# Performance work log

Measured on AMD Instinct MI355X. Metric: run time of the kernel, lower is better.

## Reference

```python
import jax, jax.numpy as jnp
import numpy as np

B, N, BS, H, DH, L, FF, V, R = 1, 4096, 64, 12, 64, 4, 3072, 30522, 3
D = H * DH
M = N // BS
NEG = -10000.0


def layernorm(x, g, b, eps=1e-5):
    mu = x.mean(-1, keepdims=True)
    var = ((x - mu) ** 2).mean(-1, keepdims=True)
    return (x - mu) * jax.lax.rsqrt(var + eps) * g + b


def bigbird_attention(q, k, v, band_mask, from_mask, to_mask, blocked_mask, rand_attn):
    # q,k,v: [b,h,n,d]; band_mask [b,1,m-4,BS,3BS]; to_mask [b,1,1,n]; from_mask [b,1,n,1]
    b, h, n, d = q.shape
    m = n // BS
    r = rand_attn.shape[-1]
    sc = 1.0 / jnp.sqrt(jnp.float32(d))
    qb = q.reshape(b, h, m, BS, d)
    kb = k.reshape(b, h, m, BS, d)
    vb = v.reshape(b, h, m, BS, d)
    hid = jnp.arange(h)[:, None, None]
    gk = kb[:, hid, rand_attn].reshape(b, h, m - 2, r * BS, d)  # gathered random keys
    gv = vb[:, hid, rand_attn].reshape(b, h, m - 2, r * BS, d)
    rand_to = blocked_mask[:, rand_attn].reshape(b, h, m - 2, r * BS)
    rand_mask = jnp.einsum('blq,bhlk->bhlqk', blocked_mask[:, 1:-1], rand_to)  # [b,h,m-2,BS,rBS]

    # first block: dense over all keys (global)
    s = jnp.einsum('bhqd,bhkd->bhqk', qb[:, :, 0], k) * sc + (1.0 - to_mask) * NEG
    c_first = jnp.einsum('bhqk,bhkd->bhqd', jax.nn.softmax(s, axis=-1), v)

    # second block: blocks 0,1,2, last, + random row 0
    k2 = jnp.concatenate([kb[:, :, 0], kb[:, :, 1], kb[:, :, 2], kb[:, :, -1], gk[:, :, 0]], axis=2)
    v2 = jnp.concatenate([vb[:, :, 0], vb[:, :, 1], vb[:, :, 2], vb[:, :, -1], gv[:, :, 0]], axis=2)
    s = jnp.einsum('bhqd,bhkd->bhqk', qb[:, :, 1], k2) * sc
    seq_pad = jnp.concatenate([to_mask[..., :3 * BS], to_mask[..., -BS:],
                               jnp.ones((b, 1, 1, r * BS), s.dtype)], axis=3)
    rnd_pad = jnp.concatenate([jnp.ones((b, h, BS, 4 * BS), s.dtype), rand_mask[:, :, 0]], axis=3)
    s = s + (1.0 - jnp.minimum(seq_pad, rnd_pad)) * NEG
    c_second = jnp.einsum('bhqk,bhkd->bhqd', jax.nn.softmax(s, axis=-1), v2)

    # middle blocks: first-global + 3-block band + random + last-global
    mq = qb[:, :, 2:-2]  # [b,h,m-4,BS,d]
    exp_k = jnp.concatenate([kb[:, :, 1:-3], kb[:, :, 2:-2], kb[:, :, 3:-1]], axis=3)
    exp_v = jnp.concatenate([vb[:, :, 1:-3], vb[:, :, 2:-2], vb[:, :, 3:-1]], axis=3)
    inner = jnp.einsum('bhlqd,bhlkd->bhlqk', mq, exp_k) * sc + (1.0 - band_mask) * NEG
    randp = jnp.einsum('bhlqd,bhlkd->bhlqk', mq, gk[:, :, 1:-1]) * sc + (1.0 - rand_mask[:, :, 1:-1]) * NEG
    firstp = jnp.einsum('bhlqd,bhkd->bhlqk', mq, kb[:, :, 0]) * sc + (1.0 - to_mask[:, :, None, :, :BS]) * NEG
    lastp = jnp.einsum('bhlqd,bhkd->bhlqk', mq, kb[:, :, -1]) * sc + (1.0 - to_mask[:, :, None, :, -BS:]) * NEG
    w = jax.nn.softmax(jnp.concatenate([firstp, inner, randp, lastp], axis=-1), axis=-1)
    c_mid = jnp.einsum('bhlqk,bhlkd->bhlqd', w[..., BS:4 * BS], exp_v)
    c_mid = c_mid + jnp.einsum('bhlqk,bhlkd->bhlqd', w[..., 4 * BS:4 * BS + r * BS], gv[:, :, 1:-1])
    c_mid = c_mid + jnp.einsum('bhlqk,bhkd->bhlqd', w[..., :BS], vb[:, :, 0])
    c_mid = c_mid + jnp.einsum('bhlqk,bhkd->bhlqd', w[..., -BS:], vb[:, :, -1])

    # second-to-last block: block 0, last 3 blocks, + random row -1
    k3 = jnp.concatenate([kb[:, :, 0], kb[:, :, -3], kb[:, :, -2], kb[:, :, -1], gk[:, :, -1]], axis=2)
    v3 = jnp.concatenate([vb[:, :, 0], vb[:, :, -3], vb[:, :, -2], vb[:, :, -1], gv[:, :, -1]], axis=2)
    s = jnp.einsum('bhqd,bhkd->bhqk', qb[:, :, -2], k3) * sc
    seq_pad = jnp.concatenate([to_mask[..., :BS], to_mask[..., -3 * BS:],
                               jnp.ones((b, 1, 1, r * BS), s.dtype)], axis=3)
    rnd_pad = jnp.concatenate([jnp.ones((b, h, BS, 4 * BS), s.dtype), rand_mask[:, :, -1]], axis=3)
    s = s + (1.0 - jnp.minimum(seq_pad, rnd_pad)) * NEG
    c_sl = jnp.einsum('bhqk,bhkd->bhqd', jax.nn.softmax(s, axis=-1), v3)

    # last block: dense over all keys (global)
    s = jnp.einsum('bhqd,bhkd->bhqk', qb[:, :, -1], k) * sc + (1.0 - to_mask) * NEG
    c_last = jnp.einsum('bhqk,bhkd->bhqd', jax.nn.softmax(s, axis=-1), v)

    ctx = jnp.concatenate([c_first[:, :, None], c_second[:, :, None], c_mid,
                           c_sl[:, :, None], c_last[:, :, None]], axis=2)
    ctx = ctx.reshape(b, h, n, d) * from_mask
    return ctx.transpose(0, 2, 1, 3).reshape(b, n, h * d)


def forward(input_ids, mask, rand_attn, emb_word, emb_pos, emb_ln_g, emb_ln_b,
            Wq, bq, Wk, bk, Wv, bv, Wo, bo, ln1_g, ln1_b, W1, b1, W2, b2, ln2_g, ln2_b):
    b, n = input_ids.shape
    m = n // BS
    x = emb_word[input_ids] + emb_pos[None, :n]
    x = layernorm(x, emb_ln_g, emb_ln_b)
    blocked_mask = mask.reshape(b, m, BS)
    exp_to = jnp.concatenate([blocked_mask[:, 1:-3], blocked_mask[:, 2:-2], blocked_mask[:, 3:-1]], axis=2)
    band_mask = jnp.einsum('blq,blk->blqk', blocked_mask[:, 2:-2], exp_to)[:, None]
    from_mask = mask.reshape(b, 1, n, 1)
    to_mask = mask.reshape(b, 1, 1, n)
    for i in range(L):
        q = (x @ Wq[i] + bq[i]).reshape(b, n, H, DH).transpose(0, 2, 1, 3)
        k = (x @ Wk[i] + bk[i]).reshape(b, n, H, DH).transpose(0, 2, 1, 3)
        v = (x @ Wv[i] + bv[i]).reshape(b, n, H, DH).transpose(0, 2, 1, 3)
        a = bigbird_attention(q, k, v, band_mask, from_mask, to_mask, blocked_mask, rand_attn)
        a = a @ Wo[i] + bo[i]
        x = layernorm(x + a, ln1_g[i], ln1_b[i])  # dropout is identity in eval
        f = jax.nn.gelu(x @ W1[i] + b1[i], approximate=False) @ W2[i] + b2[i]
        x = layernorm(x + f, ln2_g[i], ln2_b[i])
    return x


def setup_inputs() -> dict:
    key = jax.random.key(0)
    ks = jax.random.split(key, 12)
    s = 0.02
    nrm = lambda k, shape: jax.random.normal(k, shape, jnp.float32) * s
    rng = np.random.default_rng(0)
    rand_attn = jnp.asarray(rng.integers(1, M - 1, size=(H, M - 2, R)), jnp.int32)
    return {
        'input_ids': jax.random.randint(ks[0], (B, N), 0, V),
        'mask': jnp.ones((B, N), jnp.float32),
        'rand_attn': rand_attn,
        'emb_word': nrm(ks[1], (V, D)),
        'emb_pos': nrm(ks[2], (N, D)),
        'emb_ln_g': jnp.ones((D,), jnp.float32), 'emb_ln_b': jnp.zeros((D,), jnp.float32),
        'Wq': nrm(ks[3], (L, D, D)), 'bq': jnp.zeros((L, D), jnp.float32),
        'Wk': nrm(ks[4], (L, D, D)), 'bk': jnp.zeros((L, D), jnp.float32),
        'Wv': nrm(ks[5], (L, D, D)), 'bv': jnp.zeros((L, D), jnp.float32),
        'Wo': nrm(ks[6], (L, D, D)), 'bo': jnp.zeros((L, D), jnp.float32),
        'ln1_g': jnp.ones((L, D), jnp.float32), 'ln1_b': jnp.zeros((L, D), jnp.float32),
        'W1': nrm(ks[7], (L, D, FF)), 'b1': jnp.zeros((L, FF), jnp.float32),
        'W2': nrm(ks[8], (L, FF, D)), 'b2': jnp.zeros((L, D), jnp.float32),
        'ln2_g': jnp.ones((L, D), jnp.float32), 'ln2_b': jnp.zeros((L, D), jnp.float32),
    }


def reference(input_ids, mask, rand_attn, emb_word, emb_pos, emb_ln_g, emb_ln_b,
              Wq, bq, Wk, bk, Wv, bv, Wo, bo, ln1_g, ln1_b, W1, b1, W2, b2, ln2_g, ln2_b):
    return forward(input_ids, mask, rand_attn, emb_word, emb_pos, emb_ln_g, emb_ln_b,
                   Wq, bq, Wk, bk, Wv, bv, Wo, bo, ln1_g, ln1_b, W1, b1, W2, b2, ln2_g, ln2_b)
```

## Files before the change

### kernel.cpp

```cpp
#include <hip/hip_runtime.h>
#include <hip/hip_bf16.h>
#include <math.h>

#define NTOK   4096
#define DMODEL 768
#define NHEAD  12
#define DHEAD  64
#define NLAYER 4
#define DFF    3072
#define NBLK   64
#define NEGC   -10000.0f

using frag8 = __attribute__((ext_vector_type(8))) short;
using f32x4 = __attribute__((ext_vector_type(4))) float;

typedef __attribute__((address_space(3))) void       lds_void;
typedef const __attribute__((address_space(1))) void gbl_void;

__device__ __forceinline__ void gload_lds16(const void* g, void* l) {
  __builtin_amdgcn_global_load_lds((gbl_void*)g, (lds_void*)l, 16, 0, 0);
}

__device__ __forceinline__ float block_sum256(float v) {
  __shared__ float tmp[4];
  #pragma unroll
  for (int o = 32; o > 0; o >>= 1) v += __shfl_down(v, o, 64);
  __syncthreads();
  if ((threadIdx.x & 63) == 0) tmp[threadIdx.x >> 6] = v;
  __syncthreads();
  return tmp[0] + tmp[1] + tmp[2] + tmp[3];
}

__global__ __launch_bounds__(256) void embed_ln_kernel(
    const int* __restrict__ ids, const float* __restrict__ emb_word,
    const float* __restrict__ emb_pos, const float* __restrict__ g,
    const float* __restrict__ b, float* __restrict__ x,
    __hip_bfloat16* __restrict__ xb)
{
  const int n = blockIdx.x;
  const int tid = threadIdx.x;
  const int id = ids[n];
  float v[3];
  #pragma unroll
  for (int j = 0; j < 3; ++j) {
    int d = tid + j * 256;
    v[j] = emb_word[(size_t)id * DMODEL + d] + emb_pos[(size_t)n * DMODEL + d];
  }
  float mu = block_sum256(v[0] + v[1] + v[2]) * (1.0f / DMODEL);
  float var = 0.f;
  #pragma unroll
  for (int j = 0; j < 3; ++j) { float t = v[j] - mu; var += t * t; }
  var = block_sum256(var) * (1.0f / DMODEL);
  float rs = rsqrtf(var + 1e-5f);
  #pragma unroll
  for (int j = 0; j < 3; ++j) {
    int d = tid + j * 256;
    float o = (v[j] - mu) * rs * g[d] + b[d];
    x[(size_t)n * DMODEL + d] = o;
    xb[(size_t)n * DMODEL + d] = (__hip_bfloat16)o;
  }
}

__global__ __launch_bounds__(256) void add_ln_kernel(
    const float* __restrict__ xin, const float* __restrict__ o,
    const float* __restrict__ g, const float* __restrict__ b,
    float* __restrict__ dst, __hip_bfloat16* __restrict__ dstb)
{
  const int n = blockIdx.x;
  const int tid = threadIdx.x;
  float v[3];
  #pragma unroll
  for (int j = 0; j < 3; ++j) {
    int d = tid + j * 256;
    v[j] = xin[(size_t)n * DMODEL + d] + o[(size_t)n * DMODEL + d];
  }
  float mu = block_sum256(v[0] + v[1] + v[2]) * (1.0f / DMODEL);
  float var = 0.f;
  #pragma unroll
  for (int j = 0; j < 3; ++j) { float t = v[j] - mu; var += t * t; }
  var = block_sum256(var) * (1.0f / DMODEL);
  float rs = rsqrtf(var + 1e-5f);
  #pragma unroll
  for (int j = 0; j < 3; ++j) {
    int d = tid + j * 256;
    float ov = (v[j] - mu) * rs * g[d] + b[d];
    dst[(size_t)n * DMODEL + d] = ov;
    dstb[(size_t)n * DMODEL + d] = (__hip_bfloat16)ov;
  }
}

__global__ __launch_bounds__(256) void transpose_w_kernel(
    const float* __restrict__ W, __hip_bfloat16* __restrict__ WT, int K, int N)
{
  __shared__ float tile[32][33];
  const int n0 = blockIdx.x * 32;
  const int k0 = blockIdx.y * 32;
  const int c = threadIdx.x & 31;
  const int r0 = threadIdx.x >> 5;
  #pragma unroll
  for (int i = 0; i < 4; ++i) {
    int r = r0 + i * 8;
    tile[r][c] = W[(size_t)(k0 + r) * N + n0 + c];
  }
  __syncthreads();
  #pragma unroll
  for (int i = 0; i < 4; ++i) {
    int r = r0 + i * 8;
    WT[(size_t)(n0 + r) * K + k0 + c] = (__hip_bfloat16)tile[c][r];
  }
}

__global__ __launch_bounds__(256) void pack_bias_kernel(
    const float* __restrict__ bq, const float* __restrict__ bk,
    const float* __restrict__ bv, float* __restrict__ dst)
{
  int t = blockIdx.x * 256 + threadIdx.x;
  if (t < 3 * DMODEL)
    dst[t] = (t < DMODEL) ? bq[t] : (t < 2 * DMODEL ? bk[t - DMODEL] : bv[t - 2 * DMODEL]);
}

__global__ __launch_bounds__(256) void gemm_bf16_kernel(
    const __hip_bfloat16* __restrict__ A,
    const __hip_bfloat16* __restrict__ BT,
    const float* __restrict__ bias,
    float* __restrict__ Cf,
    __hip_bfloat16* __restrict__ Cb,
    int Kdim, int ldC, int do_gelu)
{
  __shared__ __hip_bfloat16 Als[2][128 * 32];
  __shared__ __hip_bfloat16 Bls[2][128 * 32];
  const int tid = threadIdx.x;
  const int bm = blockIdx.x * 128;
  const int bn = blockIdx.y * 128;

  const int wave = tid >> 6, lane = tid & 63;
  const int wm = (wave >> 1) * 64, wn = (wave & 1) * 64;
  const int lm = lane & 15, quad = lane >> 4;

  const int r0 = (0 * 4 + wave) * 16 + (lane >> 2);
  const int r1 = (1 * 4 + wave) * 16 + (lane >> 2);
  const int kc = (lane & 3) * 8;

  const __hip_bfloat16* Ar0 = A  + (size_t)(bm + r0) * Kdim + kc;
  const __hip_bfloat16* Ar1 = A  + (size_t)(bm + r1) * Kdim + kc;
  const __hip_bfloat16* Br0 = BT + (size_t)(bn + r0) * Kdim + kc;
  const __hip_bfloat16* Br1 = BT + (size_t)(bn + r1) * Kdim + kc;

  f32x4 acc[4][4];
  #pragma unroll
  for (int i = 0; i < 4; ++i)
    #pragma unroll
    for (int j = 0; j < 4; ++j)
      acc[i][j] = (f32x4){0.f, 0.f, 0.f, 0.f};

  gload_lds16(Ar0, &Als[0][r0 * 32 + kc]);
  gload_lds16(Ar1, &Als[0][r1 * 32 + kc]);
  gload_lds16(Br0, &Bls[0][r0 * 32 + kc]);
  gload_lds16(Br1, &Bls[0][r1 * 32 + kc]);

  int p = 0;
  for (int k0 = 0; k0 < Kdim; k0 += 32, p ^= 1) {
    __syncthreads();
    const int kn = k0 + 32;
    if (kn < Kdim) {
      gload_lds16(Ar0 + kn, &Als[p ^ 1][r0 * 32 + kc]);
      gload_lds16(Ar1 + kn, &Als[p ^ 1][r1 * 32 + kc]);
      gload_lds16(Br0 + kn, &Bls[p ^ 1][r0 * 32 + kc]);
      gload_lds16(Br1 + kn, &Bls[p ^ 1][r1 * 32 + kc]);
    }
    frag8 afr[4], bfr[4];
    #pragma unroll
    for (int t = 0; t < 4; ++t) {
      afr[t] = *(const frag8*)(&Als[p][(wm + t * 16 + lm) * 32 + quad * 8]);
      bfr[t] = *(const frag8*)(&Bls[p][(wn + t * 16 + lm) * 32 + quad * 8]);
    }
    #pragma unroll
    for (int mt = 0; mt < 4; ++mt)
      #pragma unroll
      for (int nt = 0; nt < 4; ++nt)
        acc[mt][nt] = __builtin_amdgcn_mfma_f32_16x16x32_bf16(
            afr[mt], bfr[nt], acc[mt][nt], 0, 0, 0);
  }

  #pragma unroll
  for (int mt = 0; mt < 4; ++mt)
    #pragma unroll
    for (int nt = 0; nt < 4; ++nt)
      #pragma unroll
      for (int r = 0; r < 4; ++r) {
        int row = bm + wm + mt * 16 + quad * 4 + r;
        int col = bn + wn + nt * 16 + lm;
        float v = acc[mt][nt][r] + bias[col];
        if (do_gelu) v = 0.5f * v * (1.f + erff(v * 0.70710678118654752f));
        if (Cf) Cf[(size_t)row * ldC + col] = v;
        if (Cb) Cb[(size_t)row * ldC + col] = (__hip_bfloat16)v;
      }
}

__global__ __launch_bounds__(256) void attn_kernel(
    const __hip_bfloat16* __restrict__ qkvb, const float* __restrict__ mask,
    const int* __restrict__ rand_attn, __hip_bfloat16* __restrict__ outp,
    float* __restrict__ Mpart, float* __restrict__ Lpart, float* __restrict__ Opart)
{
  const int h = blockIdx.x;
  const int item = blockIdx.y;
  const int tid = threadIdx.x;

  int qi, chunk;
  if (item < 8)       { qi = 0;        chunk = item; }
  else if (item < 70) { qi = item - 7; chunk = -1; }
  else                { qi = 63;       chunk = item - 70; }

  __shared__ __hip_bfloat16 Qs[64 * 72];
  __shared__ __hip_bfloat16 Ks[64 * 72];
  __shared__ __hip_bfloat16 VTs[64 * 72];
  __shared__ __hip_bfloat16 Ps[64 * 72];
  __shared__ int slist[8];
  __shared__ int snb;

  const __hip_bfloat16* qg = qkvb;
  const __hip_bfloat16* kg = qkvb + DMODEL;
  const __hip_bfloat16* vg = qkvb + 2 * DMODEL;
  const int ldq = 3 * DMODEL;

  const int wave = tid >> 6, lane = tid & 63;
  const int wm = wave * 16;
  const int lm = lane & 15, quad = lane >> 4;

  {
    int r = tid >> 2, c0 = (tid & 3) * 16;
    const __hip_bfloat16* qp = qg + (size_t)(qi * 64 + r) * ldq + h * 64 + c0;
    uint4 a = *(const uint4*)qp;
    uint4 b = *(const uint4*)(qp + 8);
    *(uint4*)(Qs + r * 72 + c0) = a;
    *(uint4*)(Qs + r * 72 + c0 + 8) = b;
  }
  if (tid == 0) {
    if (chunk >= 0) {
      for (int j = 0; j < 8; ++j) slist[j] = chunk * 8 + j;
      snb = 8;
    } else {
      const int* ra = rand_attn + ((size_t)h * 62 + (qi - 1)) * 3;
      if (qi == 1)       { slist[0] = 0; slist[1] = 1;  slist[2] = 2;  slist[3] = 63; }
      else if (qi == 62) { slist[0] = 0; slist[1] = 61; slist[2] = 62; slist[3] = 63; }
      else               { slist[0] = 0; slist[1] = qi - 1; slist[2] = qi; slist[3] = qi + 1; }
      slist[4] = ra[0]; slist[5] = ra[1]; slist[6] = ra[2];
      int nb = 7;
      if (qi >= 2 && qi <= 61) { slist[7] = 63; nb = 8; }
      snb = nb;
    }
  }
  __syncthreads();
  const int nb = snb;

  frag8 aq0 = *(const frag8*)(Qs + (wm + lm) * 72 + quad * 8);
  frag8 aq1 = *(const frag8*)(Qs + (wm + lm) * 72 + 32 + quad * 8);

  float mold[4], lsum[4];
  #pragma unroll
  for (int r = 0; r < 4; ++r) { mold[r] = -1e30f; lsum[r] = 0.f; }
  f32x4 oacc[4];
  #pragma unroll
  for (int t = 0; t < 4; ++t) oacc[t] = (f32x4){0.f, 0.f, 0.f, 0.f};

  const int sr = tid >> 2, sc0 = (tid & 3) * 16;

  for (int bi = 0; bi < nb; ++bi) {
    const int kb = slist[bi];
    const __hip_bfloat16* kp = kg + (size_t)(kb * 64 + sr) * ldq + h * 64 + sc0;
    const __hip_bfloat16* vp = vg + (size_t)(kb * 64 + sr) * ldq + h * 64 + sc0;
    uint4 kv0 = *(const uint4*)kp;
    uint4 kv1 = *(const uint4*)(kp + 8);
    uint4 vv0 = *(const uint4*)vp;
    uint4 vv1 = *(const uint4*)(vp + 8);
    float msk[4];
    #pragma unroll
    for (int t = 0; t < 4; ++t) msk[t] = mask[kb * 64 + t * 16 + lm];

    __syncthreads();
    *(uint4*)(Ks + sr * 72 + sc0) = kv0;
    *(uint4*)(Ks + sr * 72 + sc0 + 8) = kv1;
    {
      union { uint4 u[2]; __hip_bfloat16 h16[16]; } vu;
      vu.u[0] = vv0; vu.u[1] = vv1;
      #pragma unroll
      for (int j = 0; j < 16; ++j)
        VTs[(sc0 + j) * 72 + sr] = vu.h16[j];
    }
    __syncthreads();

    f32x4 sacc[4];
    #pragma unroll
    for (int t = 0; t < 4; ++t) sacc[t] = (f32x4){0.f, 0.f, 0.f, 0.f};
    #pragma unroll
    for (int t = 0; t < 4; ++t) {
      frag8 bk0 = *(const frag8*)(Ks + (t * 16 + lm) * 72 + quad * 8);
      frag8 bk1 = *(const frag8*)(Ks + (t * 16 + lm) * 72 + 32 + quad * 8);
      sacc[t] = __builtin_amdgcn_mfma_f32_16x16x32_bf16(aq0, bk0, sacc[t], 0, 0, 0);
      sacc[t] = __builtin_amdgcn_mfma_f32_16x16x32_bf16(aq1, bk1, sacc[t], 0, 0, 0);
    }

    float xs[4][4];
    #pragma unroll
    for (int t = 0; t < 4; ++t)
      #pragma unroll
      for (int r = 0; r < 4; ++r)
        xs[t][r] = sacc[t][r] * 0.125f + (1.f - msk[t]) * NEGC;

    float al[4], psum[4];
    #pragma unroll
    for (int r = 0; r < 4; ++r) {
      float rm = fmaxf(fmaxf(xs[0][r], xs[1][r]), fmaxf(xs[2][r], xs[3][r]));
      rm = fmaxf(rm, __shfl_xor(rm, 1, 64));
      rm = fmaxf(rm, __shfl_xor(rm, 2, 64));
      rm = fmaxf(rm, __shfl_xor(rm, 4, 64));
      rm = fmaxf(rm, __shfl_xor(rm, 8, 64));
      float mnew = fmaxf(mold[r], rm);
      al[r] = __expf(mold[r] - mnew);
      float s = 0.f;
      #pragma unroll
      for (int t = 0; t < 4; ++t) {
        float p = __expf(xs[t][r] - mnew);
        xs[t][r] = p;
        s += p;
      }
      s += __shfl_xor(s, 1, 64);
      s += __shfl_xor(s, 2, 64);
      s += __shfl_xor(s, 4, 64);
      s += __shfl_xor(s, 8, 64);
      psum[r] = s;
      mold[r] = mnew;
    }
    #pragma unroll
    for (int r = 0; r < 4; ++r) lsum[r] = lsum[r] * al[r] + psum[r];
    #pragma unroll
    for (int t = 0; t < 4; ++t)
      #pragma unroll
      for (int r = 0; r < 4; ++r)
        oacc[t][r] *= al[r];

    #pragma unroll
    for (int t = 0; t < 4; ++t)
      #pragma unroll
      for (int r = 0; r < 4; ++r)
        Ps[(wm + quad * 4 + r) * 72 + t * 16 + lm] = (__hip_bfloat16)xs[t][r];

    frag8 ap0 = *(const frag8*)(Ps + (wm + lm) * 72 + quad * 8);
    frag8 ap1 = *(const frag8*)(Ps + (wm + lm) * 72 + 32 + quad * 8);
    #pragma unroll
    for (int t = 0; t < 4; ++t) {
      frag8 bv0 = *(const frag8*)(VTs + (t * 16 + lm) * 72 + quad * 8);
      frag8 bv1 = *(const frag8*)(VTs + (t * 16 + lm) * 72 + 32 + quad * 8);
      oacc[t] = __builtin_amdgcn_mfma_f32_16x16x32_bf16(ap0, bv0, oacc[t], 0, 0, 0);
      oacc[t] = __builtin_amdgcn_mfma_f32_16x16x32_bf16(ap1, bv1, oacc[t], 0, 0, 0);
    }
  }

  if (chunk < 0) {
    #pragma unroll
    for (int r = 0; r < 4; ++r) {
      int row = qi * 64 + wm + quad * 4 + r;
      float sc2 = mask[row] / lsum[r];
      #pragma unroll
      for (int t = 0; t < 4; ++t)
        outp[(size_t)row * DMODEL + h * 64 + t * 16 + lm] =
            (__hip_bfloat16)(oacc[t][r] * sc2);
    }
  } else {
    const int idx = (h * 2 + (qi == 63 ? 1 : 0)) * 8 + chunk;
    #pragma unroll
    for (int r = 0; r < 4; ++r) {
      int row = wm + quad * 4 + r;
      #pragma unroll
      for (int t = 0; t < 4; ++t)
        Opart[(size_t)idx * 4096 + row * 64 + t * 16 + lm] = oacc[t][r];
      if (lm == 0) {
        Mpart[idx * 64 + row] = mold[r];
        Lpart[idx * 64 + row] = lsum[r];
      }
    }
  }
}

__global__ __launch_bounds__(256) void attn_merge_kernel(
    const float* __restrict__ Mpart, const float* __restrict__ Lpart,
    const float* __restrict__ Opart, const float* __restrict__ mask,
    __hip_bfloat16* __restrict__ outp)
{
  const int h = blockIdx.x, side = blockIdx.y;
  const int qi = side ? 63 : 0;
  const int tid = threadIdx.x;
  const int r = tid >> 2;
  const int d0 = (tid & 3) * 16;
  const int base = (h * 2 + side) * 8;

  float mv[8], m = -1e30f;
  #pragma unroll
  for (int c = 0; c < 8; ++c) { mv[c] = Mpart[(base + c) * 64 + r]; m = fmaxf(m, mv[c]); }
  float sc[8], l = 0.f;
  #pragma unroll
  for (int c = 0; c < 8; ++c) {
    sc[c] = __expf(mv[c] - m);
    l += Lpart[(base + c) * 64 + r] * sc[c];
  }
  float o[16];
  #pragma unroll
  for (int d = 0; d < 16; ++d) o[d] = 0.f;
  #pragma unroll
  for (int c = 0; c < 8; ++c) {
    const float* Op = Opart + (size_t)(base + c) * 4096 + r * 64 + d0;
    #pragma unroll
    for (int d4 = 0; d4 < 4; ++d4) {
      float4 v4 = *(const float4*)(Op + d4 * 4);
      o[d4 * 4 + 0] += v4.x * sc[c];
      o[d4 * 4 + 1] += v4.y * sc[c];
      o[d4 * 4 + 2] += v4.z * sc[c];
      o[d4 * 4 + 3] += v4.w * sc[c];
    }
  }
  const int row = qi * 64 + r;
  float inv = mask[row] / l;
  #pragma unroll
  for (int d = 0; d < 16; ++d)
    outp[(size_t)row * DMODEL + h * 64 + d0 + d] = (__hip_bfloat16)(o[d] * inv);
}

extern "C" void kernel_launch(void* const* d_in, const int* in_sizes, int n_in,
                              void* d_out, int out_size, void* d_ws, size_t ws_size,
                              hipStream_t stream)
{
  const int*   ids      = (const int*)  d_in[0];
  const float* mask     = (const float*)d_in[1];
  const int*   rand_att = (const int*)  d_in[2];
  const float* emb_word = (const float*)d_in[3];
  const float* emb_pos  = (const float*)d_in[4];
  const float* eg       = (const float*)d_in[5];
  const float* eb       = (const float*)d_in[6];
  const float* Wq = (const float*)d_in[7];
  const float* bq = (const float*)d_in[8];
  const float* Wk = (const float*)d_in[9];
  const float* bk = (const float*)d_in[10];
  const float* Wv = (const float*)d_in[11];
  const float* bv = (const float*)d_in[12];
  const float* Wo = (const float*)d_in[13];
  const float* bo = (const float*)d_in[14];
  const float* ln1g = (const float*)d_in[15];
  const float* ln1b = (const float*)d_in[16];
  const float* W1 = (const float*)d_in[17];
  const float* bf1 = (const float*)d_in[18];
  const float* W2 = (const float*)d_in[19];
  const float* bf2 = (const float*)d_in[20];
  const float* ln2g = (const float*)d_in[21];
  const float* ln2b = (const float*)d_in[22];

  const size_t ND = (size_t)NTOK * DMODEL;
  float* x   = (float*)d_ws;
  __hip_bfloat16* xb = (__hip_bfloat16*)(x + ND);
  float* t   = (float*)(xb + ND);
  __hip_bfloat16* qkvb = (__hip_bfloat16*)(t + ND);
  __hip_bfloat16* fb_b = qkvb + 3 * ND;
  __hip_bfloat16* ab_b = fb_b + (size_t)NTOK * DFF;
  __hip_bfloat16* wqkvT = ab_b + ND;
  __hip_bfloat16* woT  = wqkvT + (size_t)3 * DMODEL * DMODEL;
  __hip_bfloat16* w1T  = woT  + (size_t)DMODEL * DMODEL;
  __hip_bfloat16* w2T  = w1T  + (size_t)DFF * DMODEL;
  float* biasf = (float*)(w2T + (size_t)DMODEL * DFF);
  float* Mpart = biasf + 3 * DMODEL;
  float* Lpart = Mpart + NHEAD * 2 * 8 * 64;
  float* Opart = Lpart + NHEAD * 2 * 8 * 64;

  embed_ln_kernel<<<NTOK, 256, 0, stream>>>(ids, emb_word, emb_pos, eg, eb, x, xb);

  for (int l = 0; l < NLAYER; ++l) {
    const float* Wq_l = Wq + (size_t)l * DMODEL * DMODEL;
    const float* Wk_l = Wk + (size_t)l * DMODEL * DMODEL;
    const float* Wv_l = Wv + (size_t)l * DMODEL * DMODEL;
    const float* Wo_l = Wo + (size_t)l * DMODEL * DMODEL;
    const float* W1_l = W1 + (size_t)l * DMODEL * DFF;
    const float* W2_l = W2 + (size_t)l * DFF * DMODEL;

    dim3 g32(DMODEL / 32, DMODEL / 32);
    transpose_w_kernel<<<g32, 256, 0, stream>>>(Wq_l, wqkvT, DMODEL, DMODEL);
    transpose_w_kernel<<<g32, 256, 0, stream>>>(Wk_l, wqkvT + (size_t)DMODEL * DMODEL, DMODEL, DMODEL);
    transpose_w_kernel<<<g32, 256, 0, stream>>>(Wv_l, wqkvT + (size_t)2 * DMODEL * DMODEL, DMODEL, DMODEL);
    transpose_w_kernel<<<g32, 256, 0, stream>>>(Wo_l, woT, DMODEL, DMODEL);
    transpose_w_kernel<<<dim3(DFF / 32, DMODEL / 32), 256, 0, stream>>>(W1_l, w1T, DMODEL, DFF);
    transpose_w_kernel<<<dim3(DMODEL / 32, DFF / 32), 256, 0, stream>>>(W2_l, w2T, DFF, DMODEL);
    pack_bias_kernel<<<9, 256, 0, stream>>>(bq + (size_t)l * DMODEL, bk + (size_t)l * DMODEL,
                                            bv + (size_t)l * DMODEL, biasf);

    gemm_bf16_kernel<<<dim3(NTOK / 128, 3 * DMODEL / 128), 256, 0, stream>>>(
        xb, wqkvT, biasf, nullptr, qkvb, DMODEL, 3 * DMODEL, 0);

    attn_kernel<<<dim3(NHEAD, 78), 256, 0, stream>>>(qkvb, mask, rand_att, ab_b,
                                                     Mpart, Lpart, Opart);
    attn_merge_kernel<<<dim3(NHEAD, 2), 256, 0, stream>>>(Mpart, Lpart, Opart, mask, ab_b);

    gemm_bf16_kernel<<<dim3(NTOK / 128, DMODEL / 128), 256, 0, stream>>>(
        ab_b, woT, bo + (size_t)l * DMODEL, t, nullptr, DMODEL, DMODEL, 0);
    add_ln_kernel<<<NTOK, 256, 0, stream>>>(x, t, ln1g + (size_t)l * DMODEL,
                                            ln1b + (size_t)l * DMODEL, x, xb);

    gemm_bf16_kernel<<<dim3(NTOK / 128, DFF / 128), 256, 0, stream>>>(
        xb, w1T, bf1 + (size_t)l * DFF, nullptr, fb_b, DMODEL, DFF, 1);
    gemm_bf16_kernel<<<dim3(NTOK / 128, DMODEL / 128), 256, 0, stream>>>(
        fb_b, w2T, bf2 + (size_t)l * DMODEL, t, nullptr, DFF, DMODEL, 0);
    add_ln_kernel<<<NTOK, 256, 0, stream>>>(x, t, ln2g + (size_t)l * DMODEL,
                                            ln2b + (size_t)l * DMODEL,
                                            (l == NLAYER - 1) ? (float*)d_out : x, xb);
  }
}
```

Before: 1.154 ms.

## Split-K the narrow output GEMMs and fold partial reduction into add+LayerNorm

The Wo projection and the FFN down-projection (N=768) are split along K into 2 and 3 partitions via blockIdx.z, so each launch covers more workgroups: 192 becomes 384 and 576. Each partition writes fp32 partials to a workspace, and the add+LayerNorm kernel sums the partials and adds the bias. Previously those GEMMs launched only 32x6 tiles, which underfills the GPU's compute units. The trade-off is extra fp32 partial-buffer traffic and a slightly heavier LayerNorm kernel.

```diff
diff --git a/kernel.cpp b/kernel.cpp
--- a/kernel.cpp
+++ b/kernel.cpp
@@ -61,8 +61,9 @@
   }
 }
 
-__global__ __launch_bounds__(256) void add_ln_kernel(
-    const float* __restrict__ xin, const float* __restrict__ o,
+__global__ __launch_bounds__(256) void add_ln_red_kernel(
+    const float* __restrict__ xin, const float* __restrict__ P, size_t ps,
+    int nparts, const float* __restrict__ bias2,
     const float* __restrict__ g, const float* __restrict__ b,
     float* __restrict__ dst, __hip_bfloat16* __restrict__ dstb)
 {
@@ -72,7 +73,10 @@
   #pragma unroll
   for (int j = 0; j < 3; ++j) {
     int d = tid + j * 256;
-    v[j] = xin[(size_t)n * DMODEL + d] + o[(size_t)n * DMODEL + d];
+    float s = xin[(size_t)n * DMODEL + d] + bias2[d];
+    for (int z = 0; z < nparts; ++z)
+      s += P[(size_t)z * ps + (size_t)n * DMODEL + d];
+    v[j] = s;
   }
   float mu = block_sum256(v[0] + v[1] + v[2]) * (1.0f / DMODEL);
   float var = 0.f;
@@ -120,18 +124,20 @@
 }
 
 __global__ __launch_bounds__(256) void gemm_bf16_kernel(
-    const __hip_bfloat16* __restrict__ A,
-    const __hip_bfloat16* __restrict__ BT,
+    const __hip_bfloat16* __restrict__ A, int lda,
+    const __hip_bfloat16* __restrict__ BT, int ldb,
     const float* __restrict__ bias,
-    float* __restrict__ Cf,
+    float* __restrict__ Cf, size_t cfStride,
     __hip_bfloat16* __restrict__ Cb,
-    int Kdim, int ldC, int do_gelu)
+    int Kpart, int ldC, int do_gelu)
 {
   __shared__ __hip_bfloat16 Als[2][128 * 32];
   __shared__ __hip_bfloat16 Bls[2][128 * 32];
   const int tid = threadIdx.x;
   const int bm = blockIdx.x * 128;
   const int bn = blockIdx.y * 128;
+  const int z  = blockIdx.z;
+  const int koff = z * Kpart;
 
   const int wave = tid >> 6, lane = tid & 63;
   const int wm = (wave >> 1) * 64, wn = (wave & 1) * 64;
@@ -141,10 +147,10 @@
   const int r1 = (1 * 4 + wave) * 16 + (lane >> 2);
   const int kc = (lane & 3) * 8;
 
-  const __hip_bfloat16* Ar0 = A  + (size_t)(bm + r0) * Kdim + kc;
-  const __hip_bfloat16* Ar1 = A  + (size_t)(bm + r1) * Kdim + kc;
-  const __hip_bfloat16* Br0 = BT + (size_t)(bn + r0) * Kdim + kc;
-  const __hip_bfloat16* Br1 = BT + (size_t)(bn + r1) * Kdim + kc;
+  const __hip_bfloat16* Ar0 = A  + (size_t)(bm + r0) * lda + koff + kc;
+  const __hip_bfloat16* Ar1 = A  + (size_t)(bm + r1) * lda + koff + kc;
+  const __hip_bfloat16* Br0 = BT + (size_t)(bn + r0) * ldb + koff + kc;
+  const __hip_bfloat16* Br1 = BT + (size_t)(bn + r1) * ldb + koff + kc;
 
   f32x4 acc[4][4];
   #pragma unroll
@@ -159,10 +165,10 @@
   gload_lds16(Br1, &Bls[0][r1 * 32 + kc]);
 
   int p = 0;
-  for (int k0 = 0; k0 < Kdim; k0 += 32, p ^= 1) {
+  for (int k0 = 0; k0 < Kpart; k0 += 32, p ^= 1) {
     __syncthreads();
     const int kn = k0 + 32;
-    if (kn < Kdim) {
+    if (kn < Kpart) {
       gload_lds16(Ar0 + kn, &Als[p ^ 1][r0 * 32 + kc]);
       gload_lds16(Ar1 + kn, &Als[p ^ 1][r1 * 32 + kc]);
       gload_lds16(Br0 + kn, &Bls[p ^ 1][r0 * 32 + kc]);
@@ -182,6 +188,7 @@
             afr[mt], bfr[nt], acc[mt][nt], 0, 0, 0);
   }
 
+  float* Cfz = Cf ? Cf + (size_t)z * cfStride : nullptr;
   #pragma unroll
   for (int mt = 0; mt < 4; ++mt)
     #pragma unroll
@@ -190,9 +197,10 @@
       for (int r = 0; r < 4; ++r) {
         int row = bm + wm + mt * 16 + quad * 4 + r;
         int col = bn + wn + nt * 16 + lm;
-        float v = acc[mt][nt][r] + bias[col];
+        float v = acc[mt][nt][r];
+        if (bias) v += bias[col];
         if (do_gelu) v = 0.5f * v * (1.f + erff(v * 0.70710678118654752f));
-        if (Cf) Cf[(size_t)row * ldC + col] = v;
+        if (Cfz) Cfz[(size_t)row * ldC + col] = v;
         if (Cb) Cb[(size_t)row * ldC + col] = (__hip_bfloat16)v;
       }
 }
@@ -456,8 +464,8 @@
   const size_t ND = (size_t)NTOK * DMODEL;
   float* x   = (float*)d_ws;
   __hip_bfloat16* xb = (__hip_bfloat16*)(x + ND);
-  float* t   = (float*)(xb + ND);
-  __hip_bfloat16* qkvb = (__hip_bfloat16*)(t + ND);
+  float* P   = (float*)(xb + ND);
+  __hip_bfloat16* qkvb = (__hip_bfloat16*)(P + 3 * ND);
   __hip_bfloat16* fb_b = qkvb + 3 * ND;
   __hip_bfloat16* ab_b = fb_b + (size_t)NTOK * DFF;
   __hip_bfloat16* wqkvT = ab_b + ND;
@@ -489,24 +497,27 @@
     pack_bias_kernel<<<9, 256, 0, stream>>>(bq + (size_t)l * DMODEL, bk + (size_t)l * DMODEL,
                                             bv + (size_t)l * DMODEL, biasf);
 
-    gemm_bf16_kernel<<<dim3(NTOK / 128, 3 * DMODEL / 128), 256, 0, stream>>>(
-        xb, wqkvT, biasf, nullptr, qkvb, DMODEL, 3 * DMODEL, 0);
+    gemm_bf16_kernel<<<dim3(NTOK / 128, 3 * DMODEL / 128, 1), 256, 0, stream>>>(
+        xb, DMODEL, wqkvT, DMODEL, biasf, nullptr, 0, qkvb, DMODEL, 3 * DMODEL, 0);
 
     attn_kernel<<<dim3(NHEAD, 78), 256, 0, stream>>>(qkvb, mask, rand_att, ab_b,
                                                      Mpart, Lpart, Opart);
     attn_merge_kernel<<<dim3(NHEAD, 2), 256, 0, stream>>>(Mpart, Lpart, Opart, mask, ab_b);
 
-    gemm_bf16_kernel<<<dim3(NTOK / 128, DMODEL / 128), 256, 0, stream>>>(
-        ab_b, woT, bo + (size_t)l * DMODEL, t, nullptr, DMODEL, DMODEL, 0);
-    add_ln_kernel<<<NTOK, 256, 0, stream>>>(x, t, ln1g + (size_t)l * DMODEL,
-                                            ln1b + (size_t)l * DMODEL, x, xb);
-
-    gemm_bf16_kernel<<<dim3(NTOK / 128, DFF / 128), 256, 0, stream>>>(
-        xb, w1T, bf1 + (size_t)l * DFF, nullptr, fb_b, DMODEL, DFF, 1);
-    gemm_bf16_kernel<<<dim3(NTOK / 128, DMODEL / 128), 256, 0, stream>>>(
-        fb_b, w2T, bf2 + (size_t)l * DMODEL, t, nullptr, DFF, DMODEL, 0);
-    add_ln_kernel<<<NTOK, 256, 0, stream>>>(x, t, ln2g + (size_t)l * DMODEL,
-                                            ln2b + (size_t)l * DMODEL,
-                                            (l == NLAYER - 1) ? (float*)d_out : x, xb);
-  }
-}
+    gemm_bf16_kernel<<<dim3(NTOK / 128, DMODEL / 128, 2), 256, 0, stream>>>(
+        ab_b, DMODEL, woT, DMODEL, nullptr, P, ND, nullptr, DMODEL / 2, DMODEL, 0);
+    add_ln_red_kernel<<<NTOK, 256, 0, stream>>>(x, P, ND, 2, bo + (size_t)l * DMODEL,
+                                                ln1g + (size_t)l * DMODEL,
+                                                ln1b + (size_t)l * DMODEL, x, xb);
+
+    gemm_bf16_kernel<<<dim3(NTOK / 128, DFF / 128, 1), 256, 0, stream>>>(
+        xb, DMODEL, w1T, DMODEL, bf1 + (size_t)l * DFF, nullptr, 0, fb_b, DMODEL, DFF, 1);
+
+    gemm_bf16_kernel<<<dim3(NTOK / 128, DMODEL / 128, 3), 256, 0, stream>>>(
+        fb_b, DFF, w2T, DFF, nullptr, P, ND, nullptr, DFF / 3, DMODEL, 0);
+    add_ln_red_kernel<<<NTOK, 256, 0, stream>>>(x, P, ND, 3, bf2 + (size_t)l * DMODEL,
+                                                ln2g + (size_t)l * DMODEL,
+                                                ln2b + (size_t)l * DMODEL,
+                                                (l == NLAYER - 1) ? (float*)d_out : x, xb);
+  }
+}
```

Result: faster. 1.096 ms (-5.0%).
